# Optimization experiments

Hardware: AMD Instinct MI355X
Metric: run time of the kernel (lower is better)

## Reference

```python
import jax, jax.numpy as jnp
import numpy as np

B, N, E = 4, 4096, 2048
H_DIM = 2048
HEADS = 16
DH = H_DIM // HEADS
LN_EPS = 1e-5


def setup_inputs() -> dict:
    key = jax.random.key(0)
    ks = jax.random.split(key, 10)
    s = 1.0 / np.sqrt(E)
    so = 1.0 / np.sqrt(H_DIM)
    return {
        "x": jax.random.normal(ks[0], (B, N, E), jnp.float32),
        "Wqk": jax.random.normal(ks[1], (E, H_DIM), jnp.float32) * s,
        "bqk": jnp.zeros((H_DIM,), jnp.float32),
        "Wv": jax.random.normal(ks[2], (E, H_DIM), jnp.float32) * s,
        "bv": jnp.zeros((H_DIM,), jnp.float32),
        "Wu": jax.random.normal(ks[3], (E, H_DIM), jnp.float32) * s,
        "bu": jnp.zeros((H_DIM,), jnp.float32),
        "Wo": jax.random.normal(ks[4], (H_DIM, E), jnp.float32) * so,
        "bo": jnp.zeros((E,), jnp.float32),
        "ln_g": jnp.ones((H_DIM,), jnp.float32),
        "ln_b": jnp.zeros((H_DIM,), jnp.float32),
    }


def _heads(t):
    # [b, n, (h d)] -> [b, h, n, d]
    b, n, _ = t.shape
    return t.reshape(b, n, HEADS, DH).transpose(0, 2, 1, 3)


def _layernorm(x, g, b):
    mu = jnp.mean(x, axis=-1, keepdims=True)
    var = jnp.mean(jnp.square(x - mu), axis=-1, keepdims=True)
    return (x - mu) * jax.lax.rsqrt(var + LN_EPS) * g + b


def reference(x, Wqk, bqk, Wv, bv, Wu, bu, Wo, bo, ln_g, ln_b):
    # y = x (self-attention); qk_proj shared for q and k
    q = x @ Wqk + bqk
    k = x @ Wqk + bqk
    v = jax.nn.silu(x @ Wv + bv)   # uv_act = swish
    u = jax.nn.silu(x @ Wu + bu)
    q = jax.nn.elu(_heads(q))      # act = elu (applied after head split)
    kh = jax.nn.elu(_heads(k))
    vh = _heads(v)
    # non-causal associative form: kv = k^T v, out = q @ kv
    kv = jnp.einsum('bhnd,bhne->bhde', kh, vh)
    out = jnp.einsum('bhnd,bhde->bhne', q, kv)
    out = out.transpose(0, 2, 1, 3).reshape(x.shape[0], x.shape[1], H_DIM)
    out = _layernorm(out, ln_g, ln_b)
    out = u * out
    return out @ Wo + bo
```

## Files before the change

kernel.cpp:

```cpp
#include <hip/hip_runtime.h>

typedef __attribute__((ext_vector_type(8))) short short8;
typedef __attribute__((ext_vector_type(4))) float floatx4;

__device__ __forceinline__ float b2f(unsigned short u) {
  union { unsigned int i; float f; } c; c.i = ((unsigned int)u) << 16; return c.f;
}
__device__ __forceinline__ unsigned short f2b(float f) {
  union { float f; unsigned int i; } c; c.f = f;
  unsigned int i = c.i;
  return (unsigned short)((i + 0x7FFFu + ((i >> 16) & 1u)) >> 16);
}
__device__ __forceinline__ float elu_f(float x) {
  return x > 0.f ? x : (expf(x) - 1.f);
}
__device__ __forceinline__ float silu_f(float x) {
  return x / (1.f + expf(-x));
}
__device__ __forceinline__ void async16(const unsigned short* g, unsigned short* l) {
  __builtin_amdgcn_global_load_lds(
      (const __attribute__((address_space(1))) void*)g,
      (__attribute__((address_space(3))) void*)l, 16, 0, 0);
}
__device__ __forceinline__ floatx4 mfma16(short8 a, short8 b, floatx4 c) {
  return __builtin_amdgcn_mfma_f32_16x16x32_bf16(a, b, c, 0, 0, 0);
}

__global__ __launch_bounds__(256) void detect_dtype(
    const unsigned int* __restrict__ x, int* __restrict__ cnt) {
  int t = threadIdx.x;
  int c = 0;
  for (int i = t; i < 4096; i += 256) {
    unsigned int lo = x[i] & 0xFFFFu;
    unsigned int e = (lo >> 7) & 0xFFu;
    if (e >= 0x70u && e <= 0x8Fu) c++;
  }
#pragma unroll
  for (int off = 32; off > 0; off >>= 1) c += __shfl_down(c, off, 64);
  if ((t & 63) == 0) atomicAdd(cnt, c);
}
__device__ __forceinline__ bool is_f32(const int* flag) { return flag[0] < 2048; }

__global__ __launch_bounds__(256) void convert_x(
    const void* __restrict__ x, unsigned short* __restrict__ xb,
    const int* __restrict__ flag) {
  if (!is_f32(flag)) return;
  size_t i = ((size_t)blockIdx.x * 256 + threadIdx.x) * 8;
  const float* xf = (const float*)x;
  float4 a = *(const float4*)(xf + i);
  float4 b = *(const float4*)(xf + i + 4);
  unsigned short p[8] = {f2b(a.x), f2b(a.y), f2b(a.z), f2b(a.w),
                         f2b(b.x), f2b(b.y), f2b(b.z), f2b(b.w)};
  *(uint4*)(xb + i) = *(uint4*)p;
}

__global__ __launch_bounds__(256) void transpose2048(
    const void* __restrict__ src, unsigned short* __restrict__ dst,
    const int* __restrict__ flag) {
  const bool f32 = is_f32(flag);
  __shared__ unsigned short tile[32][33];
  int bx = blockIdx.x * 32;
  int by = blockIdx.y * 32;
  int tx = threadIdx.x & 31;
  int ty = threadIdx.x >> 5;
  for (int i = ty; i < 32; i += 8) {
    size_t idx = (size_t)(by + i) * 2048 + bx + tx;
    tile[i][tx] = f32 ? f2b(((const float*)src)[idx]) : ((const unsigned short*)src)[idx];
  }
  __syncthreads();
  for (int i = ty; i < 32; i += 8)
    dst[(size_t)(bx + i) * 2048 + by + tx] = tile[tx][i];
}

__global__ __launch_bounds__(1024) void gemm256(
    const unsigned short* __restrict__ A0,
    const unsigned short* __restrict__ A1, int a_sel,
    const unsigned short* __restrict__ WT,
    const void* __restrict__ bias,
    void* __restrict__ C, int c_ext,
    int K, int Nc, int act, const int* __restrict__ flag) {
  const bool f32 = is_f32(flag);
  const unsigned short* A = (a_sel && f32) ? A1 : A0;
  __shared__ __align__(16) unsigned short lds[8 * 8192];
#define CH(b, m, ks) (lds + ((((b)*2 + (m)) * 2 + (ks)) * 8192))
  const int nbx = gridDim.x;
  const int flat = blockIdx.y * nbx + blockIdx.x;
  const int nwg = nbx * gridDim.y;
  const int cpx = nwg >> 3;
  const int nf = (flat & 7) * cpx + (flat >> 3);
  const int bn = (nf % nbx) * 256;
  const int bm = (nf / nbx) * 256;
  const int t = threadIdx.x;
  const int lane = t & 63;
  const int wave = t >> 6;
  const int lm = lane & 15;
  const int quad = lane >> 4;
  const int wm = (wave >> 2) * 64;
  const int wn = (wave & 3) * 64;
  const int srow = lane >> 2;
  const int scol = (((lane & 3) ^ ((lane >> 3) & 3)) * 8);
  const int rq = (quad ^ ((lm >> 1) & 3)) * 8;
  const int NT = K >> 6;

  floatx4 acc[4][4] = {};

  auto stageA = [&](int kt, int ks, unsigned short* ch) {
    int rr = wave * 16;
    async16(A + (size_t)(bm + rr + srow) * K + kt + ks * 32 + scol, ch + rr * 32);
  };
  auto stageB = [&](int kt, int ks, unsigned short* ch) {
    int rr = wave * 16;
    async16(WT + (size_t)(bn + rr + srow) * K + kt + ks * 32 + scol, ch + rr * 32);
  };

  stageA(0, 0, CH(0, 0, 0));
  stageB(0, 0, CH(0, 1, 0));
  stageA(0, 1, CH(0, 0, 1));
  stageB(0, 1, CH(0, 1, 1));
  asm volatile("s_waitcnt vmcnt(0)" ::: "memory");
  asm volatile("s_barrier" ::: "memory");

  for (int ti = 0; ti < NT; ++ti) {
    const int buf = ti & 1, nb = buf ^ 1;
    const int ktn = (ti + 1 < NT ? ti + 1 : ti) << 6;

    stageA(ktn, 0, CH(nb, 0, 0));
    stageB(ktn, 0, CH(nb, 1, 0));
    stageA(ktn, 1, CH(nb, 0, 1));
    stageB(ktn, 1, CH(nb, 1, 1));

#pragma unroll
    for (int ks = 0; ks < 2; ++ks) {
      const unsigned short* cA = CH(buf, 0, ks);
      const unsigned short* cB = CH(buf, 1, ks);
      short8 af[4], bf[4];
#pragma unroll
      for (int mi = 0; mi < 4; ++mi)
        af[mi] = *(const short8*)(cA + (wm + mi * 16 + lm) * 32 + rq);
#pragma unroll
      for (int ni = 0; ni < 4; ++ni)
        bf[ni] = *(const short8*)(cB + (wn + ni * 16 + lm) * 32 + rq);
#pragma unroll
      for (int mi = 0; mi < 4; ++mi)
#pragma unroll
        for (int ni = 0; ni < 4; ++ni)
          acc[mi][ni] = mfma16(af[mi], bf[ni], acc[mi][ni]);
    }

    asm volatile("s_waitcnt vmcnt(0)" ::: "memory");
    asm volatile("s_barrier" ::: "memory");
  }

  if (c_ext && f32) {
#pragma unroll
    for (int ni = 0; ni < 4; ++ni) {
      int col = bn + wn + ni * 16 + lm;
      float bv = ((const float*)bias)[col];
#pragma unroll
      for (int mi = 0; mi < 4; ++mi) {
#pragma unroll
        for (int r = 0; r < 4; ++r) {
          int row = bm + wm + mi * 16 + quad * 4 + r;
          float v = acc[mi][ni][r] + bv;
          if (act == 1) v = silu_f(v);
          else if (act == 2) v = elu_f(v);
          ((float*)C)[(size_t)row * Nc + col] = v;
        }
      }
    }
  } else {
    unsigned short* ot = lds;
#pragma unroll
    for (int ni = 0; ni < 4; ++ni) {
      int col = wn + ni * 16 + lm;
      float bv = f32 ? ((const float*)bias)[bn + col]
                     : b2f(((const unsigned short*)bias)[bn + col]);
#pragma unroll
      for (int mi = 0; mi < 4; ++mi) {
        int rbase = wm + mi * 16 + quad * 4;
#pragma unroll
        for (int r = 0; r < 4; ++r) {
          float v = acc[mi][ni][r] + bv;
          if (act == 1) v = silu_f(v);
          else if (act == 2) v = elu_f(v);
          ot[(rbase + r) * 256 + (col ^ (quad << 4))] = f2b(v);
        }
      }
    }
    __syncthreads();
    unsigned short* Cs = (unsigned short*)C;
#pragma unroll
    for (int i = 0; i < 8; ++i) {
      int c = t + 1024 * i;
      int row = c >> 5;
      int k = c & 31;
      int phys = (k * 8) ^ (((row >> 2) & 3) << 4);
      uint4 v = *(const uint4*)&ot[row * 256 + phys];
      *(uint4*)(Cs + (size_t)(bm + row) * Nc + bn + k * 8) = v;
    }
  }
#undef CH
}

__global__ __launch_bounds__(256) void kv_accum(
    const unsigned short* __restrict__ EK,
    const unsigned short* __restrict__ V,
    float* __restrict__ kvT, int chunk) {
  const int bh = blockIdx.x;
  const int sp = blockIdx.y;
  const int b = bh >> 4, h = bh & 15;
  __shared__ __align__(16) unsigned short Kt[128][72];
  __shared__ __align__(16) unsigned short Vt[128][72];
  const int t = threadIdx.x;
  const int lane = t & 63, wave = t >> 6;
  const int lm = lane & 15, quad = lane >> 4;
  const int wm = (wave >> 1) * 64, wn = (wave & 1) * 64;
  floatx4 acc[4][4] = {};
  const size_t base = (size_t)b * 4096 * 2048 + (size_t)h * 128;
  const int nl = t & 63;
  const int dg0 = t >> 6;
  for (int n0 = sp * chunk; n0 < (sp + 1) * chunk; n0 += 64) {
#pragma unroll
    for (int i = 0; i < 4; ++i) {
      int dg = dg0 + 4 * i;
      union { uint4 u; unsigned short s[8]; } vk, vv;
      vk.u = *(const uint4*)(EK + base + (size_t)(n0 + nl) * 2048 + dg * 8);
      vv.u = *(const uint4*)(V + base + (size_t)(n0 + nl) * 2048 + dg * 8);
#pragma unroll
      for (int j = 0; j < 8; ++j) {
        Kt[dg * 8 + j][nl] = vk.s[j];
        Vt[dg * 8 + j][nl] = vv.s[j];
      }
    }
    __syncthreads();
#pragma unroll
    for (int ks = 0; ks < 2; ++ks) {
      short8 af[4], bf[4];
#pragma unroll
      for (int mi = 0; mi < 4; ++mi)
        af[mi] = *(const short8*)&Kt[wm + mi * 16 + lm][ks * 32 + quad * 8];
#pragma unroll
      for (int ni = 0; ni < 4; ++ni)
        bf[ni] = *(const short8*)&Vt[wn + ni * 16 + lm][ks * 32 + quad * 8];
#pragma unroll
      for (int mi = 0; mi < 4; ++mi)
#pragma unroll
        for (int ni = 0; ni < 4; ++ni)
          acc[mi][ni] = __builtin_amdgcn_mfma_f32_16x16x32_bf16(
              af[mi], bf[ni], acc[mi][ni], 0, 0, 0);
    }
    __syncthreads();
  }
  float* dst = kvT + (size_t)bh * 128 * 128;
#pragma unroll
  for (int mi = 0; mi < 4; ++mi)
#pragma unroll
    for (int ni = 0; ni < 4; ++ni)
#pragma unroll
      for (int r = 0; r < 4; ++r) {
        int d = wm + mi * 16 + quad * 4 + r;
        int e = wn + ni * 16 + lm;
        atomicAdd(&dst[e * 128 + d], acc[mi][ni][r]);
      }
}

__global__ __launch_bounds__(256) void attn_out(
    const unsigned short* __restrict__ EK,
    const float* __restrict__ kvT,
    unsigned short* __restrict__ O) {
  const int flat0 = blockIdx.y * 16 + blockIdx.x;
  const int nf = (flat0 & 7) * 256 + (flat0 >> 3);
  const int h = nf & 15;
  const int bm = (nf >> 4) * 128;
  const int b = bm >> 12;
  const int bh = b * 16 + h;
  __shared__ __align__(16) unsigned short As[128][136];
  __shared__ __align__(16) unsigned short Bs[128][136];
  const int t = threadIdx.x;
  const int lane = t & 63, wave = t >> 6;
  const int lm = lane & 15, quad = lane >> 4;
  const int wm = (wave >> 1) * 64, wn = (wave & 1) * 64;
  {
    const int r0 = t >> 4;
    const int g = t & 15;
#pragma unroll
    for (int i = 0; i < 8; ++i) {
      int r = r0 + 16 * i;
      uint4 vq = *(const uint4*)(EK + (size_t)(bm + r) * 2048 + h * 128 + g * 8);
      *(uint4*)&As[r][g * 8] = vq;
    }
    const int e0 = t >> 5;
    const int gg = t & 31;
    const float* kvp = kvT + (size_t)bh * 16384;
#pragma unroll
    for (int i = 0; i < 16; ++i) {
      int e = e0 + 8 * i;
      float4 f = *(const float4*)(kvp + e * 128 + gg * 4);
      unsigned short o4[4] = {f2b(f.x), f2b(f.y), f2b(f.z), f2b(f.w)};
      *(uint2*)&Bs[e][gg * 4] = *(uint2*)o4;
    }
  }
  __syncthreads();
  floatx4 acc[4][4] = {};
#pragma unroll
  for (int ks = 0; ks < 4; ++ks) {
    short8 af[4], bf[4];
#pragma unroll
    for (int mi = 0; mi < 4; ++mi)
      af[mi] = *(const short8*)&As[wm + mi * 16 + lm][ks * 32 + quad * 8];
#pragma unroll
    for (int ni = 0; ni < 4; ++ni)
      bf[ni] = *(const short8*)&Bs[wn + ni * 16 + lm][ks * 32 + quad * 8];
#pragma unroll
    for (int mi = 0; mi < 4; ++mi)
#pragma unroll
      for (int ni = 0; ni < 4; ++ni)
        acc[mi][ni] = __builtin_amdgcn_mfma_f32_16x16x32_bf16(
            af[mi], bf[ni], acc[mi][ni], 0, 0, 0);
  }
#pragma unroll
  for (int mi = 0; mi < 4; ++mi)
#pragma unroll
    for (int ni = 0; ni < 4; ++ni)
#pragma unroll
      for (int r = 0; r < 4; ++r) {
        int row = bm + wm + mi * 16 + quad * 4 + r;
        int e = wn + ni * 16 + lm;
        O[(size_t)row * 2048 + h * 128 + e] = f2b(acc[mi][ni][r]);
      }
}

__global__ __launch_bounds__(256) void ln_mul(
    const unsigned short* __restrict__ O,
    const unsigned short* __restrict__ U,
    const void* __restrict__ g,
    const void* __restrict__ bb,
    unsigned short* __restrict__ T, const int* __restrict__ flag) {
  const bool f32 = is_f32(flag);
  const int row = blockIdx.x;
  const int t = threadIdx.x;
  const size_t base = (size_t)row * 2048 + t * 8;
  union { uint4 u; unsigned short s[8]; } vo, vu;
  vo.u = *(const uint4*)(O + base);
  float vals[8];
  float s = 0.f, s2 = 0.f;
#pragma unroll
  for (int j = 0; j < 8; ++j) {
    float f = b2f(vo.s[j]);
    vals[j] = f;
    s += f;
    s2 += f * f;
  }
#pragma unroll
  for (int off = 32; off > 0; off >>= 1) {
    s += __shfl_down(s, off, 64);
    s2 += __shfl_down(s2, off, 64);
  }
  __shared__ float ps[4], ps2[4];
  int lane = t & 63, wave = t >> 6;
  if (lane == 0) { ps[wave] = s; ps2[wave] = s2; }
  __syncthreads();
  float S = ps[0] + ps[1] + ps[2] + ps[3];
  float S2 = ps2[0] + ps2[1] + ps2[2] + ps2[3];
  float mu = S * (1.f / 2048.f);
  float var = S2 * (1.f / 2048.f) - mu * mu;
  float rs = rsqrtf(var + 1e-5f);
  vu.u = *(const uint4*)(U + base);
  float gv[8], bv[8];
  if (f32) {
    float4 g0 = *(const float4*)((const float*)g + t * 8);
    float4 g1 = *(const float4*)((const float*)g + t * 8 + 4);
    float4 b0 = *(const float4*)((const float*)bb + t * 8);
    float4 b1 = *(const float4*)((const float*)bb + t * 8 + 4);
    gv[0] = g0.x; gv[1] = g0.y; gv[2] = g0.z; gv[3] = g0.w;
    gv[4] = g1.x; gv[5] = g1.y; gv[6] = g1.z; gv[7] = g1.w;
    bv[0] = b0.x; bv[1] = b0.y; bv[2] = b0.z; bv[3] = b0.w;
    bv[4] = b1.x; bv[5] = b1.y; bv[6] = b1.z; bv[7] = b1.w;
  } else {
    union { uint4 u; unsigned short s[8]; } vg, vb;
    vg.u = *(const uint4*)((const unsigned short*)g + t * 8);
    vb.u = *(const uint4*)((const unsigned short*)bb + t * 8);
#pragma unroll
    for (int j = 0; j < 8; ++j) { gv[j] = b2f(vg.s[j]); bv[j] = b2f(vb.s[j]); }
  }
  unsigned short outp[8];
#pragma unroll
  for (int j = 0; j < 8; ++j) {
    float nv = (vals[j] - mu) * rs * gv[j] + bv[j];
    outp[j] = f2b(nv * b2f(vu.s[j]));
  }
  *(uint4*)(T + base) = *(uint4*)outp;
}

extern "C" void kernel_launch(void* const* d_in, const int* in_sizes, int n_in,
                              void* d_out, int out_size, void* d_ws, size_t ws_size,
                              hipStream_t stream) {
  const void* x   = d_in[0];
  const void* Wqk = d_in[1];
  const void* bqk = d_in[2];
  const void* Wv  = d_in[3];
  const void* bv  = d_in[4];
  const void* Wu  = d_in[5];
  const void* bu  = d_in[6];
  const void* Wo  = d_in[7];
  const void* bo  = d_in[8];
  const void* lng = d_in[9];
  const void* lnb = d_in[10];

  char* ws = (char*)d_ws;
  const size_t MB = 1024 * 1024;
  int* flag = (int*)ws;
  unsigned short* WT   = (unsigned short*)(ws + 1 * MB);
  unsigned short* buf0 = (unsigned short*)(ws + 16 * MB);
  unsigned short* buf1 = (unsigned short*)(ws + 80 * MB);
  float* kvT = (float*)(ws + 144 * MB);
  unsigned short* xb = (unsigned short*)(ws + 148 * MB);

  dim3 tb(256);
  dim3 gb(1024);
  dim3 ggrid(8, 64);
  hipMemsetAsync(flag, 0, 4096, stream);
  hipMemsetAsync(kvT, 0, (size_t)64 * 128 * 128 * 4, stream);
  detect_dtype<<<1, tb, 0, stream>>>((const unsigned int*)x, flag);
  convert_x<<<16384, tb, 0, stream>>>(x, xb, flag);

  const unsigned short* xs = (const unsigned short*)x;
  transpose2048<<<dim3(64, 64), tb, 0, stream>>>(Wqk, WT, flag);
  gemm256<<<ggrid, gb, 0, stream>>>(xs, xb, 1, WT, bqk, buf0, 0, 2048, 2048, 2, flag);
  transpose2048<<<dim3(64, 64), tb, 0, stream>>>(Wv, WT, flag);
  gemm256<<<ggrid, gb, 0, stream>>>(xs, xb, 1, WT, bv, buf1, 0, 2048, 2048, 1, flag);
  kv_accum<<<dim3(64, 8), tb, 0, stream>>>(buf0, buf1, kvT, 512);
  attn_out<<<dim3(16, 128), tb, 0, stream>>>(buf0, kvT, buf1);
  transpose2048<<<dim3(64, 64), tb, 0, stream>>>(Wu, WT, flag);
  gemm256<<<ggrid, gb, 0, stream>>>(xs, xb, 1, WT, bu, buf0, 0, 2048, 2048, 1, flag);
  ln_mul<<<16384, tb, 0, stream>>>(buf1, buf0, lng, lnb, buf1, flag);
  transpose2048<<<dim3(64, 64), tb, 0, stream>>>(Wo, WT, flag);
  gemm256<<<ggrid, gb, 0, stream>>>(buf1, buf1, 0, WT, bo, d_out, 1, 2048, 2048, 0, flag);
}
```

Measured before the change: 1.024 ms.

## Emit transposed K/V from GEMM epilogue and double-buffer kv_accum with async LDS loads

The QK and V projection GEMMs now also write (or only write) a feature-major transposed copy of their output. This lets kv_accum stage K and V tiles with direct global-to-LDS async loads into a swizzled double buffer, replacing the scalar LDS transpose scatter and overlapping loads with MFMA. A separate small kernel converts the fp32 kv to bf16 once, so attn_out loads bf16 directly instead of converting per block. The cost is extra transposed global writes in the GEMM epilogue (strided 2-byte LDS gathers) and an extra 64MB workspace buffer.

```diff
diff --git a/kernel.cpp b/kernel.cpp
--- a/kernel.cpp
+++ b/kernel.cpp
@@ -78,6 +78,7 @@
     const unsigned short* __restrict__ WT,
     const void* __restrict__ bias,
     void* __restrict__ C, int c_ext,
+    unsigned short* __restrict__ CT, int wtr,
     int K, int Nc, int act, const int* __restrict__ flag) {
   const bool f32 = is_f32(flag);
   const unsigned short* A = (a_sel && f32) ? A1 : A0;
@@ -188,69 +189,101 @@
       }
     }
     __syncthreads();
-    unsigned short* Cs = (unsigned short*)C;
-#pragma unroll
-    for (int i = 0; i < 8; ++i) {
-      int c = t + 1024 * i;
-      int row = c >> 5;
-      int k = c & 31;
-      int phys = (k * 8) ^ (((row >> 2) & 3) << 4);
-      uint4 v = *(const uint4*)&ot[row * 256 + phys];
-      *(uint4*)(Cs + (size_t)(bm + row) * Nc + bn + k * 8) = v;
+    if (wtr != 2) {
+      unsigned short* Cs = (unsigned short*)C;
+#pragma unroll
+      for (int i = 0; i < 8; ++i) {
+        int c = t + 1024 * i;
+        int row = c >> 5;
+        int k = c & 31;
+        int phys = (k * 8) ^ (((row >> 2) & 3) << 4);
+        uint4 v = *(const uint4*)&ot[row * 256 + phys];
+        *(uint4*)(Cs + (size_t)(bm + row) * Nc + bn + k * 8) = v;
+      }
+    }
+    if (wtr != 0) {
+#pragma unroll
+      for (int i = 0; i < 8; ++i) {
+        int c2 = t + 1024 * i;
+        int dT = c2 >> 5;
+        int mg = c2 & 31;
+        unsigned short p[8];
+#pragma unroll
+        for (int j = 0; j < 8; ++j) {
+          int m = mg * 8 + j;
+          p[j] = ot[m * 256 + (dT ^ (((m >> 2) & 3) << 4))];
+        }
+        *(uint4*)(CT + (size_t)(bn + dT) * 16384 + bm + mg * 8) = *(uint4*)p;
+      }
     }
   }
 #undef CH
 }
 
 __global__ __launch_bounds__(256) void kv_accum(
-    const unsigned short* __restrict__ EK,
-    const unsigned short* __restrict__ V,
+    const unsigned short* __restrict__ EKT,
+    const unsigned short* __restrict__ VT,
     float* __restrict__ kvT, int chunk) {
   const int bh = blockIdx.x;
   const int sp = blockIdx.y;
   const int b = bh >> 4, h = bh & 15;
-  __shared__ __align__(16) unsigned short Kt[128][72];
-  __shared__ __align__(16) unsigned short Vt[128][72];
+  __shared__ __align__(16) unsigned short lds[8 * 4096];
+#define KCH(bu, m, ks) (lds + ((((bu)*2 + (m)) * 2 + (ks)) * 4096))
   const int t = threadIdx.x;
   const int lane = t & 63, wave = t >> 6;
   const int lm = lane & 15, quad = lane >> 4;
   const int wm = (wave >> 1) * 64, wn = (wave & 1) * 64;
+  const int srow = lane >> 2;
+  const int scol = (((lane & 3) ^ ((lane >> 3) & 3)) * 8);
+  const int rq = (quad ^ ((lm >> 1) & 3)) * 8;
   floatx4 acc[4][4] = {};
-  const size_t base = (size_t)b * 4096 * 2048 + (size_t)h * 128;
-  const int nl = t & 63;
-  const int dg0 = t >> 6;
-  for (int n0 = sp * chunk; n0 < (sp + 1) * chunk; n0 += 64) {
-#pragma unroll
-    for (int i = 0; i < 4; ++i) {
-      int dg = dg0 + 4 * i;
-      union { uint4 u; unsigned short s[8]; } vk, vv;
-      vk.u = *(const uint4*)(EK + base + (size_t)(n0 + nl) * 2048 + dg * 8);
-      vv.u = *(const uint4*)(V + base + (size_t)(n0 + nl) * 2048 + dg * 8);
-#pragma unroll
-      for (int j = 0; j < 8; ++j) {
-        Kt[dg * 8 + j][nl] = vk.s[j];
-        Vt[dg * 8 + j][nl] = vv.s[j];
-      }
-    }
-    __syncthreads();
+  const int n0base = sp * chunk + b * 4096;
+  const int NI = chunk >> 6;
+
+  auto stage = [&](const unsigned short* src, int n0, int ks, unsigned short* ch) {
+#pragma unroll
+    for (int c = 0; c < 2; ++c) {
+      int rr = c * 64 + wave * 16;
+      async16(src + (size_t)(h * 128 + rr + srow) * 16384 + n0 + ks * 32 + scol,
+              ch + rr * 32);
+    }
+  };
+
+  stage(EKT, n0base, 0, KCH(0, 0, 0));
+  stage(VT,  n0base, 0, KCH(0, 1, 0));
+  stage(EKT, n0base, 1, KCH(0, 0, 1));
+  stage(VT,  n0base, 1, KCH(0, 1, 1));
+  asm volatile("s_waitcnt vmcnt(0)" ::: "memory");
+  asm volatile("s_barrier" ::: "memory");
+
+  for (int ti = 0; ti < NI; ++ti) {
+    const int buf = ti & 1, nb = buf ^ 1;
+    const int nn = n0base + ((ti + 1 < NI ? ti + 1 : ti) << 6);
+    stage(EKT, nn, 0, KCH(nb, 0, 0));
+    stage(VT,  nn, 0, KCH(nb, 1, 0));
+    stage(EKT, nn, 1, KCH(nb, 0, 1));
+    stage(VT,  nn, 1, KCH(nb, 1, 1));
 #pragma unroll
     for (int ks = 0; ks < 2; ++ks) {
+      const unsigned short* cA = KCH(buf, 0, ks);
+      const unsigned short* cB = KCH(buf, 1, ks);
       short8 af[4], bf[4];
 #pragma unroll
       for (int mi = 0; mi < 4; ++mi)
-        af[mi] = *(const short8*)&Kt[wm + mi * 16 + lm][ks * 32 + quad * 8];
+        af[mi] = *(const short8*)(cA + (wm + mi * 16 + lm) * 32 + rq);
 #pragma unroll
       for (int ni = 0; ni < 4; ++ni)
-        bf[ni] = *(const short8*)&Vt[wn + ni * 16 + lm][ks * 32 + quad * 8];
+        bf[ni] = *(const short8*)(cB + (wn + ni * 16 + lm) * 32 + rq);
 #pragma unroll
       for (int mi = 0; mi < 4; ++mi)
 #pragma unroll
         for (int ni = 0; ni < 4; ++ni)
-          acc[mi][ni] = __builtin_amdgcn_mfma_f32_16x16x32_bf16(
-              af[mi], bf[ni], acc[mi][ni], 0, 0, 0);
-    }
-    __syncthreads();
-  }
+          acc[mi][ni] = mfma16(af[mi], bf[ni], acc[mi][ni]);
+    }
+    asm volatile("s_waitcnt vmcnt(0)" ::: "memory");
+    asm volatile("s_barrier" ::: "memory");
+  }
+
   float* dst = kvT + (size_t)bh * 128 * 128;
 #pragma unroll
   for (int mi = 0; mi < 4; ++mi)
@@ -262,11 +295,22 @@
         int e = wn + ni * 16 + lm;
         atomicAdd(&dst[e * 128 + d], acc[mi][ni][r]);
       }
+#undef KCH
+}
+
+__global__ __launch_bounds__(256) void kv_to_bf16(
+    const float* __restrict__ kvT, unsigned short* __restrict__ kvb) {
+  size_t i = ((size_t)blockIdx.x * 256 + threadIdx.x) * 8;
+  float4 a = *(const float4*)(kvT + i);
+  float4 b = *(const float4*)(kvT + i + 4);
+  unsigned short p[8] = {f2b(a.x), f2b(a.y), f2b(a.z), f2b(a.w),
+                         f2b(b.x), f2b(b.y), f2b(b.z), f2b(b.w)};
+  *(uint4*)(kvb + i) = *(uint4*)p;
 }
 
 __global__ __launch_bounds__(256) void attn_out(
     const unsigned short* __restrict__ EK,
-    const float* __restrict__ kvT,
+    const unsigned short* __restrict__ kvb,
     unsigned short* __restrict__ O) {
   const int flat0 = blockIdx.y * 16 + blockIdx.x;
   const int nf = (flat0 & 7) * 256 + (flat0 >> 3);
@@ -289,15 +333,12 @@
       uint4 vq = *(const uint4*)(EK + (size_t)(bm + r) * 2048 + h * 128 + g * 8);
       *(uint4*)&As[r][g * 8] = vq;
     }
-    const int e0 = t >> 5;
-    const int gg = t & 31;
-    const float* kvp = kvT + (size_t)bh * 16384;
-#pragma unroll
-    for (int i = 0; i < 16; ++i) {
-      int e = e0 + 8 * i;
-      float4 f = *(const float4*)(kvp + e * 128 + gg * 4);
-      unsigned short o4[4] = {f2b(f.x), f2b(f.y), f2b(f.z), f2b(f.w)};
-      *(uint2*)&Bs[e][gg * 4] = *(uint2*)o4;
+    const unsigned short* kvp = kvb + (size_t)bh * 16384;
+#pragma unroll
+    for (int i = 0; i < 8; ++i) {
+      int c = t + 256 * i;
+      int e = c >> 4, g2 = c & 15;
+      *(uint4*)&Bs[e][g2 * 8] = *(const uint4*)(kvp + e * 128 + g2 * 8);
     }
   }
   __syncthreads();
@@ -411,10 +452,12 @@
   const size_t MB = 1024 * 1024;
   int* flag = (int*)ws;
   unsigned short* WT   = (unsigned short*)(ws + 1 * MB);
+  unsigned short* kvb  = (unsigned short*)(ws + 12 * MB);
   unsigned short* buf0 = (unsigned short*)(ws + 16 * MB);
   unsigned short* buf1 = (unsigned short*)(ws + 80 * MB);
   float* kvT = (float*)(ws + 144 * MB);
-  unsigned short* xb = (unsigned short*)(ws + 148 * MB);
+  unsigned short* xb  = (unsigned short*)(ws + 148 * MB);
+  unsigned short* EKT = (unsigned short*)(ws + 212 * MB);
 
   dim3 tb(256);
   dim3 gb(1024);
@@ -426,14 +469,15 @@
 
   const unsigned short* xs = (const unsigned short*)x;
   transpose2048<<<dim3(64, 64), tb, 0, stream>>>(Wqk, WT, flag);
-  gemm256<<<ggrid, gb, 0, stream>>>(xs, xb, 1, WT, bqk, buf0, 0, 2048, 2048, 2, flag);
+  gemm256<<<ggrid, gb, 0, stream>>>(xs, xb, 1, WT, bqk, buf0, 0, EKT, 1, 2048, 2048, 2, flag);
   transpose2048<<<dim3(64, 64), tb, 0, stream>>>(Wv, WT, flag);
-  gemm256<<<ggrid, gb, 0, stream>>>(xs, xb, 1, WT, bv, buf1, 0, 2048, 2048, 1, flag);
-  kv_accum<<<dim3(64, 8), tb, 0, stream>>>(buf0, buf1, kvT, 512);
-  attn_out<<<dim3(16, 128), tb, 0, stream>>>(buf0, kvT, buf1);
+  gemm256<<<ggrid, gb, 0, stream>>>(xs, xb, 1, WT, bv, buf1, 0, buf1, 2, 2048, 2048, 1, flag);
+  kv_accum<<<dim3(64, 8), tb, 0, stream>>>(EKT, buf1, kvT, 512);
+  kv_to_bf16<<<512, tb, 0, stream>>>(kvT, kvb);
+  attn_out<<<dim3(16, 128), tb, 0, stream>>>(buf0, kvb, buf1);
   transpose2048<<<dim3(64, 64), tb, 0, stream>>>(Wu, WT, flag);
-  gemm256<<<ggrid, gb, 0, stream>>>(xs, xb, 1, WT, bu, buf0, 0, 2048, 2048, 1, flag);
+  gemm256<<<ggrid, gb, 0, stream>>>(xs, xb, 1, WT, bu, buf0, 0, EKT, 0, 2048, 2048, 1, flag);
   ln_mul<<<16384, tb, 0, stream>>>(buf1, buf0, lng, lnb, buf1, flag);
   transpose2048<<<dim3(64, 64), tb, 0, stream>>>(Wo, WT, flag);
-  gemm256<<<ggrid, gb, 0, stream>>>(buf1, buf1, 0, WT, bo, d_out, 1, 2048, 2048, 0, flag);
-}
+  gemm256<<<ggrid, gb, 0, stream>>>(buf1, buf1, 0, WT, bo, d_out, 1, EKT, 0, 2048, 2048, 0, flag);
+}
```

New measurement: 1.082 ms. +5.7%, slower.
